# Performance work log

Measured on AMD Instinct MI355X. Metric: run time of the kernel, lower is better.

Reference implementation:

```python
import jax, jax.numpy as jnp
import numpy as np

N_ORB = 1024    # Monte-Carlo orbits
NTIMES = 1024   # observation epochs
N_FZ = 24       # zodi flux grid points (uniform in log10)
N_KEZ = 6       # exozodi multipliers (sorted, searchsorted lookup)
N_TINT = 64     # integration times
N_ALPHA = 512   # separations (uniform in log10)


def setup_inputs() -> dict:
    key = jax.random.key(0)
    k1, k2, k3, k4 = jax.random.split(key, 4)
    fZs = jnp.logspace(-10.0, -7.0, N_FZ).astype(jnp.float32)
    alphas = jnp.logspace(-2.0, 1.0, N_ALPHA).astype(jnp.float32)
    kEZs = jnp.array([0.5, 1.0, 2.0, 5.0, 10.0, 20.0], dtype=jnp.float32)
    # grid already in the module's internal (n_fZ, n_kEZ, n_tint, n_alpha) layout
    grid = 25.0 + jax.random.normal(k1, (N_FZ, N_KEZ, N_TINT, N_ALPHA), dtype=jnp.float32)
    # alpha slightly exceeds [alphas[0], alphas[-1]] so geom_mask is exercised
    alpha = (10.0 ** jax.random.uniform(k2, (N_ORB, NTIMES), minval=-2.2, maxval=1.1)).astype(jnp.float32)
    dMag = (25.0 + jax.random.normal(k3, (N_ORB, NTIMES))).astype(jnp.float32)
    fZ_vals = (10.0 ** jax.random.uniform(k4, (NTIMES,), minval=-10.0, maxval=-7.0)).astype(jnp.float32)
    kEZ_val = jnp.float32(1.5)
    return dict(alpha=alpha, dMag=dMag, fZ_vals=fZ_vals, kEZ_val=kEZ_val,
                grid=grid, fZs=fZs, kEZs=kEZs, alphas=alphas)


def reference(alpha, dMag, fZ_vals, kEZ_val, grid, fZs, kEZs, alphas):
    """Faithful vectorized translation of dMag0Grid._pdet_alpha_dMag.

    alpha, dMag: (n_orb, ntimes); fZ_vals: (ntimes,); kEZ_val: scalar;
    grid: (n_fZ, n_kEZ, n_tint, n_alpha). Returns pdet (ntimes, n_tint).
    """
    n_fZ = fZs.shape[0]
    n_alpha = alphas.shape[0]
    log_fZs = jnp.log10(fZs)
    inv_log_fZ_step = 1.0 / (log_fZs[1] - log_fZs[0])
    log_alphas = jnp.log10(alphas)
    inv_log_alpha_step = 1.0 / (log_alphas[1] - log_alphas[0])

    geom_mask = (alpha >= alphas[0]) & (alpha <= alphas[-1])          # (n_orb, ntimes)

    fZ_ind = (jnp.log10(fZ_vals) - log_fZs[0]) * inv_log_fZ_step
    fZ0 = jnp.clip(jnp.floor(fZ_ind).astype(jnp.int32) + 1, 0, n_fZ - 2)  # (ntimes,)

    a_ind = (jnp.log10(alpha) - log_alphas[0]) * inv_log_alpha_step
    a0 = jnp.clip(a_ind.astype(jnp.int32), 0, n_alpha - 1)               # (n_orb, ntimes)
    dalpha = (a_ind - a0).astype(grid.dtype)

    kEZ_ind = jnp.searchsorted(kEZs, kEZ_val, side='right') - 1

    # lax.dynamic_slice clamps the start so the width-2 window fits:
    s = jnp.minimum(a0, n_alpha - 2)                                     # (n_orb, ntimes)

    g = jnp.take(grid, kEZ_ind, axis=1)                                  # (n_fZ, n_tint, n_alpha)
    g_f = g[fZ0]                                                          # (ntimes, n_tint, n_alpha)
    sT = s.T                                                              # (ntimes, n_orb)
    g0 = jnp.take_along_axis(g_f, sT[:, None, :], axis=2)                 # (ntimes, n_tint, n_orb)
    g1 = jnp.take_along_axis(g_f, (sT + 1)[:, None, :], axis=2)
    res = g0 + dalpha.T[:, None, :] * (g1 - g0)                           # (ntimes, n_tint, n_orb)

    dim = jnp.transpose(res, (2, 0, 1))                                   # (n_orb, ntimes, n_tint)
    det_mask = geom_mask[..., None] & jnp.signbit(dMag[..., None] - dim)
    pdet = det_mask.astype(jnp.float32).mean(axis=0)                      # (ntimes, n_tint)
    return pdet
```

## Files before the change

kernel.cpp:

```cpp
#include <hip/hip_runtime.h>
#include <math.h>

#define N_ORB   1024
#define NTIMES  1024
#define N_FZ    24
#define N_KEZ   6
#define N_TINT  64
#define N_ALPHA 512

#define SL_STRIDE 34

#define GT_BYTES (N_FZ * N_ALPHA * N_TINT * 4)

__global__ __launch_bounds__(256) void stage_inputs(
    const float* __restrict__ grid, const float* __restrict__ kEZs,
    const float* __restrict__ kEZ_val_p, const float* __restrict__ alpha,
    const float* __restrict__ dMag, const float* __restrict__ alphas,
    float* __restrict__ gT, float2* __restrict__ Pc)
{
    __shared__ float lds[64 * 65];

    int b = blockIdx.x;
    if (b < 192) {
        float kv = kEZ_val_p[0];
        int cnt = 0;
#pragma unroll
        for (int i = 0; i < N_KEZ; ++i) cnt += (kEZs[i] <= kv) ? 1 : 0;
        int kez = cnt - 1;
        kez = kez < 0 ? 0 : (kez > N_KEZ - 1 ? N_KEZ - 1 : kez);

        int fz = b >> 3, sc = b & 7;
        int w = threadIdx.x >> 6, lane = threadIdx.x & 63;
        const float* gsrc = grid + ((size_t)fz * N_KEZ + kez) * N_TINT * N_ALPHA;

#pragma unroll
        for (int r = 0; r < 16; ++r) {
            int tint = w * 16 + r;
            lds[tint * 65 + lane] = gsrc[(size_t)tint * N_ALPHA + sc * 64 + lane];
        }
        __syncthreads();
#pragma unroll
        for (int r = 0; r < 16; ++r) {
            int sl = w * 16 + r;
            gT[((size_t)fz * N_ALPHA + sc * 64 + sl) * N_TINT + lane] = lds[lane * 65 + sl];
        }
    } else {
        float* ut = lds;
        float* dt = lds + 1056;

        int u = b - 192;
        int t0 = (u & 31) * 32, o0 = (u >> 5) * 32;
        int row = threadIdx.x >> 5, col = threadIdx.x & 31;

        float al0 = alphas[0], al1 = alphas[N_ALPHA - 1];
        float la0 = log10f(al0);
        float inv_step = 1.0f / (log10f(alphas[1]) - la0);

#pragma unroll
        for (int r = 0; r < 4; ++r) {
            int ol = r * 8 + row;
            size_t idx = (size_t)(o0 + ol) * NTIMES + t0 + col;
            float a = alpha[idx];
            float d = dMag[idx];
            float a_ind = (log10f(a) - la0) * inv_step;
            int a0i = (int)a_ind;
            a0i = a0i < 0 ? 0 : (a0i > N_ALPHA - 1 ? N_ALPHA - 1 : a0i);
            float dal = a_ind - (float)a0i;
            int s = a0i > N_ALPHA - 2 ? N_ALPHA - 2 : a0i;
            bool geom = (a >= al0) && (a <= al1);
            float uv = (float)s + dal;
            uv = fminf(fmaxf(uv, 0.0f), 510.999f);
            if (!geom) uv = 0.0f;
            ut[ol * 33 + col] = uv;
            dt[ol * 33 + col] = geom ? d : __builtin_inff();
        }
        __syncthreads();
#pragma unroll
        for (int r = 0; r < 4; ++r) {
            int tl = r * 8 + row;
            float2 v;
            v.x = ut[col * 33 + tl];
            v.y = dt[col * 33 + tl];
            Pc[(size_t)(t0 + tl) * N_ORB + o0 + col] = v;
        }
    }
}

__global__ __launch_bounds__(256) void pdet_main(
    const float* __restrict__ fZ_vals, const float* __restrict__ fZs,
    const float* __restrict__ gT, const float2* __restrict__ Pc,
    float* __restrict__ out)
{
    __shared__ float sl[N_ALPHA * SL_STRIDE];
    __shared__ int   red[4 * 32];

    int t = blockIdx.x >> 1;
    int h = blockIdx.x & 1;
    int tid = threadIdx.x;

    float lf0 = log10f(fZs[0]);
    float inv_f = 1.0f / (log10f(fZs[1]) - lf0);
    float fi = (log10f(fZ_vals[t]) - lf0) * inv_f;
    int f0 = (int)floorf(fi) + 1;
    f0 = f0 < 0 ? 0 : (f0 > N_FZ - 2 ? N_FZ - 2 : f0);

    const float*  gB = gT + (size_t)f0 * N_ALPHA * N_TINT + h * 32;
    const float2* Pt = Pc + (size_t)t * N_ORB;

#pragma unroll
    for (int it = 0; it < 16; ++it) {
        int idx = it * 256 + tid;
        int s = idx >> 3, jj = idx & 7;
        float4 g = *reinterpret_cast<const float4*>(gB + (size_t)s * N_TINT + jj * 4);
        float* dst = &sl[s * SL_STRIDE + jj * 4];
        dst[0] = g.x; dst[1] = g.y; dst[2] = g.z; dst[3] = g.w;
    }
    __syncthreads();

    int w = tid >> 6, lane = tid & 63;
    int o  = lane >> 4;
    int tp = lane & 15;
    int tb = tp * 2;

    const float2* Pw = Pt + w * 256 + o;

    int c0 = 0, c1 = 0;

#pragma unroll 8
    for (int k = 0; k < 64; ++k) {
        float2 p = Pw[k * 4];
        float u = p.x, dm = p.y;
        int su = (int)u;
        float fr = u - (float)su;
        const float* r = &sl[su * SL_STRIDE + tb];
        float g00 = r[0];
        float g01 = r[1];
        float g10 = r[SL_STRIDE];
        float g11 = r[SL_STRIDE + 1];
        c0 += dm < fmaf(fr, g10 - g00, g00);
        c1 += dm < fmaf(fr, g11 - g01, g01);
    }

    c0 += __shfl_xor(c0, 16); c0 += __shfl_xor(c0, 32);
    c1 += __shfl_xor(c1, 16); c1 += __shfl_xor(c1, 32);
    if (lane < 16) {
        red[w * 32 + tp * 2]     = c0;
        red[w * 32 + tp * 2 + 1] = c1;
    }
    __syncthreads();
    if (tid < 32) {
        int tot = red[tid] + red[32 + tid] + red[64 + tid] + red[96 + tid];
        out[(size_t)t * N_TINT + h * 32 + tid] = (float)tot * (1.0f / 1024.0f);
    }
}

extern "C" void kernel_launch(void* const* d_in, const int* in_sizes, int n_in,
                              void* d_out, int out_size, void* d_ws, size_t ws_size,
                              hipStream_t stream) {
    const float* alpha   = (const float*)d_in[0];
    const float* dMag    = (const float*)d_in[1];
    const float* fZ_vals = (const float*)d_in[2];
    const float* kEZ_val = (const float*)d_in[3];
    const float* grid    = (const float*)d_in[4];
    const float* fZs     = (const float*)d_in[5];
    const float* kEZs    = (const float*)d_in[6];
    const float* alphas  = (const float*)d_in[7];
    float*  out = (float*)d_out;

    float*  gT = (float*)d_ws;
    float2* Pc = (float2*)((char*)d_ws + GT_BYTES);

    stage_inputs<<<dim3(192 + 1024), 256, 0, stream>>>(
        grid, kEZs, kEZ_val, alpha, dMag, alphas, gT, Pc);
    pdet_main<<<dim3(NTIMES * 2), 256, 0, stream>>>(fZ_vals, fZs, gT, Pc, out);
}
```

Baseline: 112.3 us.

## Bucket epochs by fZ index so each block reuses its staged grid slice

Adds a single-block counting sort that groups time epochs by their fZ grid index and writes a sorted index list. The main kernel now launches a quarter as many blocks, each processing four consecutive sorted epochs, and reloads the LDS grid slice only when the fZ index changes. This targets the repeated global-to-LDS load of the same grid slice for epochs that share an fZ bin. In exchange it adds a serialized sort block and extra barriers, and it reduces block-level parallelism, which may lower occupancy and latency hiding.

```diff
diff --git a/kernel.cpp b/kernel.cpp
--- a/kernel.cpp
+++ b/kernel.cpp
@@ -11,16 +11,19 @@
 #define SL_STRIDE 34
 
 #define GT_BYTES (N_FZ * N_ALPHA * N_TINT * 4)
+#define PC_BYTES (NTIMES * N_ORB * 8)
 
 __global__ __launch_bounds__(256) void stage_inputs(
     const float* __restrict__ grid, const float* __restrict__ kEZs,
     const float* __restrict__ kEZ_val_p, const float* __restrict__ alpha,
     const float* __restrict__ dMag, const float* __restrict__ alphas,
-    float* __restrict__ gT, float2* __restrict__ Pc)
+    const float* __restrict__ fZ_vals, const float* __restrict__ fZs,
+    float* __restrict__ gT, float2* __restrict__ Pc, int* __restrict__ tOrdF)
 {
     __shared__ float lds[64 * 65];
 
     int b = blockIdx.x;
+    int tid = threadIdx.x;
     if (b < 192) {
         float kv = kEZ_val_p[0];
         int cnt = 0;
@@ -30,7 +33,7 @@
         kez = kez < 0 ? 0 : (kez > N_KEZ - 1 ? N_KEZ - 1 : kez);
 
         int fz = b >> 3, sc = b & 7;
-        int w = threadIdx.x >> 6, lane = threadIdx.x & 63;
+        int w = tid >> 6, lane = tid & 63;
         const float* gsrc = grid + ((size_t)fz * N_KEZ + kez) * N_TINT * N_ALPHA;
 
 #pragma unroll
@@ -44,13 +47,13 @@
             int sl = w * 16 + r;
             gT[((size_t)fz * N_ALPHA + sc * 64 + sl) * N_TINT + lane] = lds[lane * 65 + sl];
         }
-    } else {
+    } else if (b < 1216) {
         float* ut = lds;
         float* dt = lds + 1056;
 
         int u = b - 192;
         int t0 = (u & 31) * 32, o0 = (u >> 5) * 32;
-        int row = threadIdx.x >> 5, col = threadIdx.x & 31;
+        int row = tid >> 5, col = tid & 31;
 
         float al0 = alphas[0], al1 = alphas[N_ALPHA - 1];
         float la0 = log10f(al0);
@@ -83,74 +86,105 @@
             v.y = dt[col * 33 + tl];
             Pc[(size_t)(t0 + tl) * N_ORB + o0 + col] = v;
         }
+    } else {
+        int* ih   = (int*)lds;
+        int* base = (int*)lds + 32;
+        if (tid < 32) ih[tid] = 0;
+        __syncthreads();
+
+        float lf0 = log10f(fZs[0]);
+        float inv_f = 1.0f / (log10f(fZs[1]) - lf0);
+        int f0v[4], tv[4];
+#pragma unroll
+        for (int k = 0; k < 4; ++k) {
+            int t = k * 256 + tid;
+            float fi = (log10f(fZ_vals[t]) - lf0) * inv_f;
+            int f0 = (int)floorf(fi) + 1;
+            f0 = f0 < 0 ? 0 : (f0 > N_FZ - 2 ? N_FZ - 2 : f0);
+            f0v[k] = f0; tv[k] = t;
+            atomicAdd(&ih[f0], 1);
+        }
+        __syncthreads();
+        if (tid == 0) {
+            int run = 0;
+#pragma unroll
+            for (int j = 0; j < 23; ++j) { base[j] = run; run += ih[j]; }
+        }
+        __syncthreads();
+#pragma unroll
+        for (int k = 0; k < 4; ++k) {
+            int pos = atomicAdd(&base[f0v[k]], 1);
+            tOrdF[pos] = (f0v[k] << 10) | tv[k];
+        }
     }
 }
 
 __global__ __launch_bounds__(256) void pdet_main(
-    const float* __restrict__ fZ_vals, const float* __restrict__ fZs,
-    const float* __restrict__ gT, const float2* __restrict__ Pc,
-    float* __restrict__ out)
+    const int* __restrict__ tOrdF, const float* __restrict__ gT,
+    const float2* __restrict__ Pc, float* __restrict__ out)
 {
     __shared__ float sl[N_ALPHA * SL_STRIDE];
-    __shared__ int   red[4 * 32];
-
-    int t = blockIdx.x >> 1;
-    int h = blockIdx.x & 1;
+    __shared__ int   red[128];
+
+    int bb = blockIdx.x >> 1;
+    int h  = blockIdx.x & 1;
     int tid = threadIdx.x;
-
-    float lf0 = log10f(fZs[0]);
-    float inv_f = 1.0f / (log10f(fZs[1]) - lf0);
-    float fi = (log10f(fZ_vals[t]) - lf0) * inv_f;
-    int f0 = (int)floorf(fi) + 1;
-    f0 = f0 < 0 ? 0 : (f0 > N_FZ - 2 ? N_FZ - 2 : f0);
-
-    const float*  gB = gT + (size_t)f0 * N_ALPHA * N_TINT + h * 32;
-    const float2* Pt = Pc + (size_t)t * N_ORB;
-
-#pragma unroll
-    for (int it = 0; it < 16; ++it) {
-        int idx = it * 256 + tid;
-        int s = idx >> 3, jj = idx & 7;
-        float4 g = *reinterpret_cast<const float4*>(gB + (size_t)s * N_TINT + jj * 4);
-        float* dst = &sl[s * SL_STRIDE + jj * 4];
-        dst[0] = g.x; dst[1] = g.y; dst[2] = g.z; dst[3] = g.w;
-    }
-    __syncthreads();
-
     int w = tid >> 6, lane = tid & 63;
     int o  = lane >> 4;
     int tp = lane & 15;
-    int tb = tp * 2;
-
-    const float2* Pw = Pt + w * 256 + o;
-
-    int c0 = 0, c1 = 0;
+
+    int curF0 = -1;
+
+    for (int i = 0; i < 4; ++i) {
+        int e  = tOrdF[bb * 4 + i];
+        int t  = e & 1023;
+        int f0 = e >> 10;
+
+        if (f0 != curF0) {
+            __syncthreads();
+            const float* gB = gT + (size_t)f0 * N_ALPHA * N_TINT + h * 32;
+#pragma unroll
+            for (int it = 0; it < 16; ++it) {
+                int idx = it * 256 + tid;
+                int s = idx >> 3, jj = idx & 7;
+                float4 g = *reinterpret_cast<const float4*>(gB + (size_t)s * N_TINT + jj * 4);
+                float* dst = &sl[s * SL_STRIDE + jj * 4];
+                dst[0] = g.x; dst[1] = g.y; dst[2] = g.z; dst[3] = g.w;
+            }
+            __syncthreads();
+            curF0 = f0;
+        }
+
+        const float2* Pg = Pc + (size_t)t * N_ORB + w * 256 + o;
+        int c0 = 0, c1 = 0;
 
 #pragma unroll 8
-    for (int k = 0; k < 64; ++k) {
-        float2 p = Pw[k * 4];
-        float u = p.x, dm = p.y;
-        int su = (int)u;
-        float fr = u - (float)su;
-        const float* r = &sl[su * SL_STRIDE + tb];
-        float g00 = r[0];
-        float g01 = r[1];
-        float g10 = r[SL_STRIDE];
-        float g11 = r[SL_STRIDE + 1];
-        c0 += dm < fmaf(fr, g10 - g00, g00);
-        c1 += dm < fmaf(fr, g11 - g01, g01);
-    }
-
-    c0 += __shfl_xor(c0, 16); c0 += __shfl_xor(c0, 32);
-    c1 += __shfl_xor(c1, 16); c1 += __shfl_xor(c1, 32);
-    if (lane < 16) {
-        red[w * 32 + tp * 2]     = c0;
-        red[w * 32 + tp * 2 + 1] = c1;
-    }
-    __syncthreads();
-    if (tid < 32) {
-        int tot = red[tid] + red[32 + tid] + red[64 + tid] + red[96 + tid];
-        out[(size_t)t * N_TINT + h * 32 + tid] = (float)tot * (1.0f / 1024.0f);
+        for (int k = 0; k < 64; ++k) {
+            float2 p = Pg[k * 4];
+            float u = p.x, dm = p.y;
+            int su = (int)u;
+            float fr = u - (float)su;
+            const float* r = &sl[su * SL_STRIDE + tp * 2];
+            float g00 = r[0];
+            float g01 = r[1];
+            float g10 = r[SL_STRIDE];
+            float g11 = r[SL_STRIDE + 1];
+            c0 += dm < fmaf(fr, g10 - g00, g00);
+            c1 += dm < fmaf(fr, g11 - g01, g01);
+        }
+
+        c0 += __shfl_xor(c0, 16); c0 += __shfl_xor(c0, 32);
+        c1 += __shfl_xor(c1, 16); c1 += __shfl_xor(c1, 32);
+        if (lane < 16) {
+            red[w * 32 + tp * 2]     = c0;
+            red[w * 32 + tp * 2 + 1] = c1;
+        }
+        __syncthreads();
+        if (tid < 32) {
+            int tot = red[tid] + red[32 + tid] + red[64 + tid] + red[96 + tid];
+            out[(size_t)t * N_TINT + h * 32 + tid] = (float)tot * (1.0f / 1024.0f);
+        }
+        __syncthreads();
     }
 }
 
@@ -167,10 +201,11 @@
     const float* alphas  = (const float*)d_in[7];
     float*  out = (float*)d_out;
 
-    float*  gT = (float*)d_ws;
-    float2* Pc = (float2*)((char*)d_ws + GT_BYTES);
-
-    stage_inputs<<<dim3(192 + 1024), 256, 0, stream>>>(
-        grid, kEZs, kEZ_val, alpha, dMag, alphas, gT, Pc);
-    pdet_main<<<dim3(NTIMES * 2), 256, 0, stream>>>(fZ_vals, fZs, gT, Pc, out);
+    float*  gT    = (float*)d_ws;
+    float2* Pc    = (float2*)((char*)d_ws + GT_BYTES);
+    int*    tOrdF = (int*)((char*)d_ws + GT_BYTES + PC_BYTES);
+
+    stage_inputs<<<dim3(1217), 256, 0, stream>>>(
+        grid, kEZs, kEZ_val, alpha, dMag, alphas, fZ_vals, fZs, gT, Pc, tOrdF);
+    pdet_main<<<dim3(512), 256, 0, stream>>>(tOrdF, gT, Pc, out);
 }
```

Result: faster. 109.8 us (-2.3%).
